# Optimization experiments

Measured on AMD Instinct MI355X. Metric: run time of the kernel, lower is better.

## Reference

```python
import math
import jax, jax.numpy as jnp
import numpy as np

EMB = 1024
HEADS = 16
HEAD_DIM = EMB // HEADS
FF = 4 * EMB
EPS = 1e-5


def gelu_tanh(x):
    c = math.sqrt(2.0 / math.pi)
    return 0.5 * x * (1.0 + jnp.tanh(c * (x + 0.044715 * x ** 3)))


def layernorm(x, scale, shift):
    mean = jnp.mean(x, axis=-1, keepdims=True)
    var = jnp.var(x, axis=-1, keepdims=True)
    return scale * (x - mean) / jnp.sqrt(var + EPS) + shift


def setup_inputs() -> dict:
    key = jax.random.key(0)
    ks = jax.random.split(key, 10)
    s = 0.02
    return {
        "x": jax.random.normal(ks[0], (2, 2048, EMB), dtype=jnp.float32),
        "Wq": jax.random.normal(ks[1], (EMB, EMB), dtype=jnp.float32) * s,
        "Wk": jax.random.normal(ks[2], (EMB, EMB), dtype=jnp.float32) * s,
        "Wv": jax.random.normal(ks[3], (EMB, EMB), dtype=jnp.float32) * s,
        "Wo": jax.random.normal(ks[4], (EMB, EMB), dtype=jnp.float32) * s,
        "bo": jnp.zeros((EMB,), dtype=jnp.float32),
        "W1": jax.random.normal(ks[5], (EMB, FF), dtype=jnp.float32) * s,
        "b1": jnp.zeros((FF,), dtype=jnp.float32),
        "W2": jax.random.normal(ks[6], (FF, EMB), dtype=jnp.float32) * s,
        "b2": jnp.zeros((EMB,), dtype=jnp.float32),
        "ln1_scale": jnp.ones((EMB,), dtype=jnp.float32),
        "ln1_shift": jnp.zeros((EMB,), dtype=jnp.float32),
        "ln2_scale": jnp.ones((EMB,), dtype=jnp.float32),
        "ln2_shift": jnp.zeros((EMB,), dtype=jnp.float32),
    }


def reference(x, Wq, Wk, Wv, Wo, bo, W1, b1, W2, b2,
              ln1_scale, ln1_shift, ln2_scale, ln2_shift):
    B, S, D = x.shape
    # --- pre-LN causal MHA ---
    h = layernorm(x, ln1_scale, ln1_shift)
    q = (h @ Wq).reshape(B, S, HEADS, HEAD_DIM).transpose(0, 2, 1, 3)  # [B,H,S,d]
    k = (h @ Wk).reshape(B, S, HEADS, HEAD_DIM).transpose(0, 2, 1, 3)
    v = (h @ Wv).reshape(B, S, HEADS, HEAD_DIM).transpose(0, 2, 1, 3)
    scores = jnp.einsum("bhqd,bhkd->bhqk", q, k)  # [B,H,S,S]
    causal = jnp.triu(jnp.ones((S, S), dtype=bool), k=1)
    scores = jnp.where(causal, -jnp.inf, scores)
    attn = jax.nn.softmax(scores / math.sqrt(HEAD_DIM), axis=-1)
    ctx = jnp.einsum("bhqk,bhkd->bhqd", attn, v)  # [B,H,S,d]
    ctx = ctx.transpose(0, 2, 1, 3).reshape(B, S, D)
    x = x + (ctx @ Wo + bo)
    # --- FFN ---
    h = layernorm(x, ln2_scale, ln2_shift)
    h = gelu_tanh(h @ W1 + b1) @ W2 + b2
    return x + h
```

## Files before the change

### kernel.cpp

```cpp
#include <hip/hip_runtime.h>
#include <hip/hip_bf16.h>
#include <math.h>

#define EMB 1024
#define HEADS 16
#define HEAD_DIM 64
#define FF_DIM 4096
#define SEQ 2048
#define BATCH 2
#define NTOK (BATCH * SEQ)
#define LN_EPS 1e-5f
#define QKV_N 3072
#define Q_PRESCALE 0.18033688011112042f

typedef __attribute__((ext_vector_type(8))) short s8v;
typedef __attribute__((ext_vector_type(4))) float f4v;

__device__ __forceinline__ unsigned short f2bf(float f) {
    union { __hip_bfloat16 h; unsigned short u; } cv;
    cv.h = __float2bfloat16(f);
    return cv.u;
}

__device__ __forceinline__ float fast_exp2(float x) {
#if __has_builtin(__builtin_amdgcn_exp2f)
    return __builtin_amdgcn_exp2f(x);
#else
    return exp2f(x);
#endif
}

__device__ __forceinline__ float gelu_f(float x) {
    const float c = 0.7978845608028654f;
    float x3 = x * x * x;
    return 0.5f * x * (1.0f + tanhf(c * (x + 0.044715f * x3)));
}

#define GLDS(gp, lp)                                                        \
    __builtin_amdgcn_global_load_lds(                                       \
        (const __attribute__((address_space(1))) void*)(gp),                \
        (__attribute__((address_space(3))) void*)(lp), 16, 0, 0)

__global__ __launch_bounds__(256) void ln_bf16_kernel(const float* __restrict__ x,
                                                      const float* __restrict__ scale,
                                                      const float* __restrict__ shift,
                                                      unsigned short* __restrict__ out) {
    int row = blockIdx.x;
    int tid = threadIdx.x;
    const float4 xv = ((const float4*)(x + (size_t)row * EMB))[tid];
    float s  = xv.x + xv.y + xv.z + xv.w;
    float ss = xv.x * xv.x + xv.y * xv.y + xv.z * xv.z + xv.w * xv.w;
    __shared__ float2 red[256];
    red[tid] = make_float2(s, ss);
    __syncthreads();
    for (int off = 128; off > 0; off >>= 1) {
        if (tid < off) {
            red[tid].x += red[tid + off].x;
            red[tid].y += red[tid + off].y;
        }
        __syncthreads();
    }
    float mean = red[0].x * (1.0f / EMB);
    float var  = red[0].y * (1.0f / EMB) - mean * mean;
    float rstd = rsqrtf(var + LN_EPS);
    float4 sc4 = ((const float4*)scale)[tid];
    float4 sh4 = ((const float4*)shift)[tid];
    ushort4 o;
    o.x = f2bf(sc4.x * (xv.x - mean) * rstd + sh4.x);
    o.y = f2bf(sc4.y * (xv.y - mean) * rstd + sh4.y);
    o.z = f2bf(sc4.z * (xv.z - mean) * rstd + sh4.z);
    o.w = f2bf(sc4.w * (xv.w - mean) * rstd + sh4.w);
    *(ushort4*)(out + (size_t)row * EMB + tid * 4) = o;
}

__global__ __launch_bounds__(256) void tconv_kernel(const float* __restrict__ W,
                                                    unsigned short* __restrict__ Wt,
                                                    int K, int N) {
    __shared__ float t[64][65];
    int n0 = blockIdx.x * 64, k0 = blockIdx.y * 64;
    int tid = threadIdx.x;
#pragma unroll
    for (int it = 0; it < 4; ++it) {
        int f = tid + it * 256;
        int r = f >> 4, c = (f & 15) * 4;
        float4 w = *(const float4*)(W + (size_t)(k0 + r) * N + n0 + c);
        t[r][c] = w.x; t[r][c + 1] = w.y; t[r][c + 2] = w.z; t[r][c + 3] = w.w;
    }
    __syncthreads();
#pragma unroll
    for (int it = 0; it < 4; ++it) {
        int f = tid + it * 256;
        int rn = f >> 4, ck = (f & 15) * 4;
        ushort4 o;
        o.x = f2bf(t[ck + 0][rn]);
        o.y = f2bf(t[ck + 1][rn]);
        o.z = f2bf(t[ck + 2][rn]);
        o.w = f2bf(t[ck + 3][rn]);
        *(ushort4*)(Wt + (size_t)(n0 + rn) * K + k0 + ck) = o;
    }
}

__global__ __launch_bounds__(256) void reduce_kernel(const float* __restrict__ p0,
                                                     const float* __restrict__ p1,
                                                     const float* __restrict__ bias,
                                                     const float* __restrict__ residual,
                                                     float* __restrict__ out) {
    size_t i4 = ((size_t)blockIdx.x * 256 + threadIdx.x) * 4;
    float4 a = *(const float4*)(p0 + i4);
    float4 b = *(const float4*)(p1 + i4);
    float4 r = *(const float4*)(residual + i4);
    int col = (int)(i4 & (EMB - 1));
    float4 bs = *(const float4*)(bias + col);
    float4 o;
    o.x = a.x + b.x + r.x + bs.x;
    o.y = a.y + b.y + r.y + bs.y;
    o.z = a.z + b.z + r.z + bs.z;
    o.w = a.w + b.w + r.w + bs.w;
    *(float4*)(out + i4) = o;
}

__global__ __launch_bounds__(256) void reduce_ln_kernel(const float* __restrict__ p0,
                                                        const float* __restrict__ p1,
                                                        const float* __restrict__ bias,
                                                        const float* __restrict__ residual,
                                                        float* __restrict__ x1,
                                                        const float* __restrict__ scale,
                                                        const float* __restrict__ shift,
                                                        unsigned short* __restrict__ out) {
    int row = blockIdx.x;
    int tid = threadIdx.x;
    size_t i4 = (size_t)row * EMB + tid * 4;
    float4 a = *(const float4*)(p0 + i4);
    float4 b = *(const float4*)(p1 + i4);
    float4 r = *(const float4*)(residual + i4);
    float4 bs = *(const float4*)(bias + tid * 4);
    float4 xv;
    xv.x = a.x + b.x + r.x + bs.x;
    xv.y = a.y + b.y + r.y + bs.y;
    xv.z = a.z + b.z + r.z + bs.z;
    xv.w = a.w + b.w + r.w + bs.w;
    *(float4*)(x1 + i4) = xv;

    float s  = xv.x + xv.y + xv.z + xv.w;
    float ss = xv.x * xv.x + xv.y * xv.y + xv.z * xv.z + xv.w * xv.w;
    __shared__ float2 red[256];
    red[tid] = make_float2(s, ss);
    __syncthreads();
    for (int off = 128; off > 0; off >>= 1) {
        if (tid < off) {
            red[tid].x += red[tid + off].x;
            red[tid].y += red[tid + off].y;
        }
        __syncthreads();
    }
    float mean = red[0].x * (1.0f / EMB);
    float var  = red[0].y * (1.0f / EMB) - mean * mean;
    float rstd = rsqrtf(var + LN_EPS);
    float4 sc4 = ((const float4*)scale)[tid];
    float4 sh4 = ((const float4*)shift)[tid];
    ushort4 o;
    o.x = f2bf(sc4.x * (xv.x - mean) * rstd + sh4.x);
    o.y = f2bf(sc4.y * (xv.y - mean) * rstd + sh4.y);
    o.z = f2bf(sc4.z * (xv.z - mean) * rstd + sh4.z);
    o.w = f2bf(sc4.w * (xv.w - mean) * rstd + sh4.w);
    *(ushort4*)(out + i4) = o;
}

__global__ __launch_bounds__(256) void gemm_bf16_kernel(
    const unsigned short* __restrict__ A,
    const unsigned short* __restrict__ Bt,
    float* __restrict__ Cf0,
    float* __restrict__ Cf1,
    unsigned short* __restrict__ Cb,
    int M, int N, int K, int Klen,
    const float* __restrict__ bias,
    const float* __restrict__ residual,
    int do_gelu, int qkv_mode,
    unsigned short* __restrict__ vt)
{
    __shared__ short As[2][4096];
    __shared__ short Bs[2][4096];

    int tid = threadIdx.x;
    int m0 = blockIdx.y * 128;
    int n0 = blockIdx.x * 128;
    int k0 = blockIdx.z * Klen;
    float* Cf = blockIdx.z ? Cf1 : Cf0;
    int wv = tid >> 6, lane = tid & 63;
    int wr = wv >> 1, wc = wv & 1;
    int quad = lane >> 4, ln = lane & 15;

    f4v acc[4][4];
#pragma unroll
    for (int i = 0; i < 4; ++i)
#pragma unroll
        for (int j = 0; j < 4; ++j) {
            f4v z = {0.f, 0.f, 0.f, 0.f};
            acc[i][j] = z;
        }

    int r0 = tid & 127;
    size_t Kby = (size_t)K << 1;
    const char* Ag0 = (const char*)A + (size_t)(m0 + r0) * Kby + (size_t)k0 * 2 + (tid >> 7) * 16;
    const char* Bg0 = (const char*)Bt + (size_t)(n0 + r0) * Kby + (size_t)k0 * 2 + (tid >> 7) * 16;

    int nIter = Klen >> 5;
    GLDS(Ag0, (char*)As[0] + tid * 16);
    GLDS(Ag0 + 32, (char*)As[0] + tid * 16 + 4096);
    GLDS(Bg0, (char*)Bs[0] + tid * 16);
    GLDS(Bg0 + 32, (char*)Bs[0] + tid * 16 + 4096);

    for (int it = 0; it < nIter; ++it) {
        __syncthreads();
        if (it + 1 < nIter) {
            int kb = (it + 1) << 6;
            char* Ad = (char*)As[(it + 1) & 1] + tid * 16;
            char* Bd = (char*)Bs[(it + 1) & 1] + tid * 16;
            GLDS(Ag0 + kb, Ad);
            GLDS(Ag0 + kb + 32, Ad + 4096);
            GLDS(Bg0 + kb, Bd);
            GLDS(Bg0 + kb + 32, Bd + 4096);
        }
        const short* Ab = As[it & 1];
        const short* Bb = Bs[it & 1];
        s8v af[4], bfr[4];
#pragma unroll
        for (int i = 0; i < 4; ++i)
            af[i] = *(const s8v*)(Ab + ((size_t)quad * 128 + wr * 64 + i * 16 + ln) * 8);
#pragma unroll
        for (int j = 0; j < 4; ++j)
            bfr[j] = *(const s8v*)(Bb + ((size_t)quad * 128 + wc * 64 + j * 16 + ln) * 8);
#pragma unroll
        for (int i = 0; i < 4; ++i)
#pragma unroll
            for (int j = 0; j < 4; ++j)
                acc[i][j] = __builtin_amdgcn_mfma_f32_16x16x32_bf16(af[i], bfr[j], acc[i][j], 0, 0, 0);
    }

    int cn  = n0 + wc * 64 + ln;
    int cm0 = m0 + wr * 64 + quad * 4;

    if (qkv_mode) {
        if (n0 < 2048) {
            float sc = (n0 < 1024) ? Q_PRESCALE : 1.0f;
#pragma unroll
            for (int j = 0; j < 4; ++j) {
                int gn = cn + j * 16;
#pragma unroll
                for (int i = 0; i < 4; ++i)
#pragma unroll
                    for (int r = 0; r < 4; ++r)
                        Cb[(size_t)(cm0 + i * 16 + r) * 2048 + gn] = f2bf(acc[i][j][r] * sc);
            }
        } else {
#pragma unroll
            for (int j = 0; j < 4; ++j) {
                int gn = cn + j * 16 - 2048;
#pragma unroll
                for (int i = 0; i < 4; ++i) {
                    int gm0 = cm0 + i * 16;
                    int bb = gm0 >> 11, s0 = gm0 & 2047;
                    ushort4 pk;
                    pk.x = f2bf(acc[i][j][0]);
                    pk.y = f2bf(acc[i][j][1]);
                    pk.z = f2bf(acc[i][j][2]);
                    pk.w = f2bf(acc[i][j][3]);
                    *(ushort4*)(vt + ((size_t)bb * 1024 + gn) * SEQ + s0) = pk;
                }
            }
        }
        return;
    }

#pragma unroll
    for (int j = 0; j < 4; ++j) {
        int gn = cn + j * 16;
        float bj = bias ? bias[gn] : 0.f;
#pragma unroll
        for (int i = 0; i < 4; ++i) {
#pragma unroll
            for (int r = 0; r < 4; ++r) {
                int gm = cm0 + i * 16 + r;
                float vv = acc[i][j][r] + bj;
                if (do_gelu) vv = gelu_f(vv);
                if (residual) vv += residual[(size_t)gm * N + gn];
                if (Cf) Cf[(size_t)gm * N + gn] = vv;
                else    Cb[(size_t)gm * N + gn] = f2bf(vv);
            }
        }
    }
}

__global__ __launch_bounds__(256) void flash_attn_mfma_kernel(
    const unsigned short* __restrict__ qk,
    const unsigned short* __restrict__ vt,
    unsigned short* __restrict__ ctx)
{
    int h  = blockIdx.x;
    int qt = (int)gridDim.y - 1 - (int)blockIdx.y;
    int b  = blockIdx.z;
    int tid = threadIdx.x;
    int w = tid >> 6, lane = tid & 63;
    int quad = lane >> 4, ln = lane & 15;

    __shared__ short Kb2[2][4096];
    __shared__ short Vb2[2][4096];
    __shared__ short Ps[4][32 * 72];

    size_t qrow0 = (size_t)b * SEQ + (size_t)qt * 128;
    int wrow0 = w * 32;

    s8v qf[2][2];
#pragma unroll
    for (int mb = 0; mb < 2; ++mb)
#pragma unroll
        for (int ks = 0; ks < 2; ++ks)
            qf[mb][ks] = *(const s8v*)(qk + (qrow0 + wrow0 + mb * 16 + ln) * 2048
                                          + h * 64 + ks * 32 + quad * 8);

    float l_part[2][4];
    f4v o[2][4];
#pragma unroll
    for (int mb = 0; mb < 2; ++mb) {
#pragma unroll
        for (int r = 0; r < 4; ++r) l_part[mb][r] = 0.f;
#pragma unroll
        for (int db = 0; db < 4; ++db) {
            f4v z = {0.f, 0.f, 0.f, 0.f};
            o[mb][db] = z;
        }
    }

    const unsigned short* kb_p = qk + (size_t)b * SEQ * 2048 + 1024 + h * 64;
    const unsigned short* vb_p = vt + ((size_t)b * 1024 + h * 64) * SEQ;
    short* Pw = Ps[w];

    int rr = tid & 63;
    const unsigned short* Kg0 = kb_p + (size_t)rr * 2048 + (tid >> 6) * 8;
    const unsigned short* Vg0 = vb_p + (size_t)rr * 2048 + (tid >> 6) * 8;

    int ktn = 2 * qt + 2;
    int ktmax_w = (qt * 128 + wrow0 + 31) >> 6;

    GLDS(Kg0, (char*)Kb2[0] + tid * 16);
    GLDS(Kg0 + 32, (char*)Kb2[0] + tid * 16 + 4096);
    GLDS(Vg0, (char*)Vb2[0] + tid * 16);
    GLDS(Vg0 + 32, (char*)Vb2[0] + tid * 16 + 4096);

    for (int kt = 0; kt < ktn; ++kt) {
        __syncthreads();
        if (kt + 1 < ktn) {
            int nb_ = (kt + 1) & 1;
            const unsigned short* ks_ = Kg0 + (size_t)(kt + 1) * 64 * 2048;
            const unsigned short* vs_ = Vg0 + (kt + 1) * 64;
            GLDS(ks_, (char*)Kb2[nb_] + tid * 16);
            GLDS(ks_ + 32, (char*)Kb2[nb_] + tid * 16 + 4096);
            GLDS(vs_, (char*)Vb2[nb_] + tid * 16);
            GLDS(vs_ + 32, (char*)Vb2[nb_] + tid * 16 + 4096);
        }
        if (kt > ktmax_w) continue;

        const short* Kl = Kb2[kt & 1];
        const short* Vl = Vb2[kt & 1];

        f4v s[2][4];
#pragma unroll
        for (int mb = 0; mb < 2; ++mb)
#pragma unroll
            for (int nb = 0; nb < 4; ++nb) {
                f4v z = {0.f, 0.f, 0.f, 0.f};
                s[mb][nb] = z;
            }
#pragma unroll
        for (int ks = 0; ks < 2; ++ks)
#pragma unroll
            for (int nb = 0; nb < 4; ++nb) {
                s8v kfr = *(const s8v*)(Kl + ((size_t)(ks * 4 + quad) * 64 + nb * 16 + ln) * 8);
#pragma unroll
                for (int mb = 0; mb < 2; ++mb)
                    s[mb][nb] = __builtin_amdgcn_mfma_f32_16x16x32_bf16(qf[mb][ks], kfr, s[mb][nb], 0, 0, 0);
            }

#pragma unroll
        for (int mb = 0; mb < 2; ++mb) {
#pragma unroll
            for (int r = 0; r < 4; ++r) {
                int rloc = mb * 16 + quad * 4 + r;
                int grow = qt * 128 + wrow0 + rloc;
                float p[4];
#pragma unroll
                for (int nb = 0; nb < 4; ++nb) {
                    int key = kt * 64 + nb * 16 + ln;
                    float e = fast_exp2(s[mb][nb][r]);
                    p[nb] = (key > grow) ? 0.f : e;
                }
                l_part[mb][r] += (p[0] + p[1]) + (p[2] + p[3]);
#pragma unroll
                for (int nb = 0; nb < 4; ++nb)
                    Pw[rloc * 72 + nb * 16 + ln] = f2bf(p[nb]);
            }
        }

#pragma unroll
        for (int ks = 0; ks < 2; ++ks) {
            s8v pf[2];
#pragma unroll
            for (int mb = 0; mb < 2; ++mb)
                pf[mb] = *(const s8v*)(Pw + (mb * 16 + ln) * 72 + ks * 32 + quad * 8);
#pragma unroll
            for (int db = 0; db < 4; ++db) {
                s8v vfr = *(const s8v*)(Vl + ((size_t)(ks * 4 + quad) * 64 + db * 16 + ln) * 8);
#pragma unroll
                for (int mb = 0; mb < 2; ++mb)
                    o[mb][db] = __builtin_amdgcn_mfma_f32_16x16x32_bf16(pf[mb], vfr, o[mb][db], 0, 0, 0);
            }
        }
    }

#pragma unroll
    for (int mb = 0; mb < 2; ++mb)
#pragma unroll
        for (int r = 0; r < 4; ++r) {
            float l = l_part[mb][r];
#pragma unroll
            for (int msk = 1; msk < 16; msk <<= 1)
                l += __shfl_xor(l, msk);
            float inv = 1.0f / l;
            size_t row = qrow0 + wrow0 + mb * 16 + quad * 4 + r;
#pragma unroll
            for (int db = 0; db < 4; ++db)
                ctx[row * EMB + h * 64 + db * 16 + ln] = f2bf(o[mb][db][r] * inv);
        }
}

extern "C" void kernel_launch(void* const* d_in, const int* in_sizes, int n_in,
                              void* d_out, int out_size, void* d_ws, size_t ws_size,
                              hipStream_t stream) {
    const float* x    = (const float*)d_in[0];
    const float* Wq   = (const float*)d_in[1];
    const float* Wk   = (const float*)d_in[2];
    const float* Wv   = (const float*)d_in[3];
    const float* Wo   = (const float*)d_in[4];
    const float* bo   = (const float*)d_in[5];
    const float* W1   = (const float*)d_in[6];
    const float* b1   = (const float*)d_in[7];
    const float* W2   = (const float*)d_in[8];
    const float* b2   = (const float*)d_in[9];
    const float* ln1s = (const float*)d_in[10];
    const float* ln1b = (const float*)d_in[11];
    const float* ln2s = (const float*)d_in[12];
    const float* ln2b = (const float*)d_in[13];
    float* out = (float*)d_out;

    const size_t MiB = 1024 * 1024;
    uint8_t* w8 = (uint8_t*)d_ws;
    unsigned short* Wqkv_t = (unsigned short*)(w8);
    unsigned short* Wo_t   = (unsigned short*)(w8 +  6 * MiB);
    unsigned short* W1_t   = (unsigned short*)(w8 +  8 * MiB);
    unsigned short* W2_t   = (unsigned short*)(w8 + 16 * MiB);
    unsigned short* act_bf = (unsigned short*)(w8 + 24 * MiB);
    unsigned short* qk_bf  = (unsigned short*)(w8 + 32 * MiB);
    unsigned short* vt     = (unsigned short*)(w8 + 48 * MiB);
    float*          p0a    = (float*)(w8 + 32 * MiB);
    float*          p1a    = (float*)(w8 + 48 * MiB);
    unsigned short* u_bf   = (unsigned short*)(w8 + 32 * MiB);
    float*          x1     = (float*)(w8 + 64 * MiB);
    float*          p0b    = (float*)(w8);
    float*          p1b    = (float*)(w8 + 80 * MiB);

    tconv_kernel<<<dim3(16, 16), 256, 0, stream>>>(Wq, Wqkv_t, EMB, EMB);
    tconv_kernel<<<dim3(16, 16), 256, 0, stream>>>(Wk, Wqkv_t + (size_t)1024 * EMB, EMB, EMB);
    tconv_kernel<<<dim3(16, 16), 256, 0, stream>>>(Wv, Wqkv_t + (size_t)2048 * EMB, EMB, EMB);
    tconv_kernel<<<dim3(16, 16), 256, 0, stream>>>(Wo, Wo_t, EMB, EMB);
    tconv_kernel<<<dim3(64, 16), 256, 0, stream>>>(W1, W1_t, EMB, FF_DIM);
    tconv_kernel<<<dim3(16, 64), 256, 0, stream>>>(W2, W2_t, FF_DIM, EMB);

    ln_bf16_kernel<<<NTOK, 256, 0, stream>>>(x, ln1s, ln1b, act_bf);

    gemm_bf16_kernel<<<dim3(QKV_N / 128, NTOK / 128, 1), 256, 0, stream>>>(
        act_bf, Wqkv_t, nullptr, nullptr, qk_bf, NTOK, QKV_N, EMB, EMB,
        nullptr, nullptr, 0, 1, vt);

    flash_attn_mfma_kernel<<<dim3(HEADS, SEQ / 128, BATCH), 256, 0, stream>>>(qk_bf, vt, act_bf);

    gemm_bf16_kernel<<<dim3(EMB / 128, NTOK / 128, 2), 256, 0, stream>>>(
        act_bf, Wo_t, p0a, p1a, nullptr, NTOK, EMB, EMB, 512,
        nullptr, nullptr, 0, 0, nullptr);
    reduce_ln_kernel<<<NTOK, 256, 0, stream>>>(p0a, p1a, bo, x, x1, ln2s, ln2b, act_bf);

    gemm_bf16_kernel<<<dim3(FF_DIM / 128, NTOK / 128, 1), 256, 0, stream>>>(
        act_bf, W1_t, nullptr, nullptr, u_bf, NTOK, FF_DIM, EMB, EMB,
        b1, nullptr, 1, 0, nullptr);

    gemm_bf16_kernel<<<dim3(EMB / 128, NTOK / 128, 2), 256, 0, stream>>>(
        u_bf, W2_t, p0b, p1b, nullptr, NTOK, EMB, FF_DIM, 2048,
        nullptr, nullptr, 0, 0, nullptr);
    reduce_kernel<<<(NTOK * EMB) / 1024, 256, 0, stream>>>(p0b, p1b, b2, x1, out);
}
```

Measured before the change: 493.3 us.

## Add 128x256 wide GEMM for QKV/FFN1, merge weight transposes, specialize split-K GEMM

```diff
diff --git a/kernel.cpp b/kernel.cpp
--- a/kernel.cpp
+++ b/kernel.cpp
@@ -73,12 +73,11 @@
     *(ushort4*)(out + (size_t)row * EMB + tid * 4) = o;
 }
 
-__global__ __launch_bounds__(256) void tconv_kernel(const float* __restrict__ W,
-                                                    unsigned short* __restrict__ Wt,
-                                                    int K, int N) {
+__device__ __forceinline__ void tconv_tile(const float* __restrict__ W,
+                                           unsigned short* __restrict__ Wt,
+                                           int K, int N, int bx, int by, int tid) {
     __shared__ float t[64][65];
-    int n0 = blockIdx.x * 64, k0 = blockIdx.y * 64;
-    int tid = threadIdx.x;
+    int n0 = bx * 64, k0 = by * 64;
 #pragma unroll
     for (int it = 0; it < 4; ++it) {
         int f = tid + it * 256;
@@ -98,6 +97,22 @@
         o.w = f2bf(t[ck + 3][rn]);
         *(ushort4*)(Wt + (size_t)(n0 + rn) * K + k0 + ck) = o;
     }
+}
+
+__global__ __launch_bounds__(256) void tconv_all_kernel(
+    const float* __restrict__ Wq, const float* __restrict__ Wk,
+    const float* __restrict__ Wv, const float* __restrict__ Wo,
+    const float* __restrict__ W1, const float* __restrict__ W2,
+    unsigned short* __restrict__ Wqkv_t, unsigned short* __restrict__ Wo_t,
+    unsigned short* __restrict__ W1_t, unsigned short* __restrict__ W2_t) {
+    int b = blockIdx.x;
+    int tid = threadIdx.x;
+    if (b < 256)        tconv_tile(Wq, Wqkv_t,                      EMB, EMB,    b & 15, b >> 4, tid);
+    else if (b < 512)   tconv_tile(Wk, Wqkv_t + (size_t)1024 * EMB, EMB, EMB,    (b - 256) & 15, (b - 256) >> 4, tid);
+    else if (b < 768)   tconv_tile(Wv, Wqkv_t + (size_t)2048 * EMB, EMB, EMB,    (b - 512) & 15, (b - 512) >> 4, tid);
+    else if (b < 1024)  tconv_tile(Wo, Wo_t,                        EMB, EMB,    (b - 768) & 15, (b - 768) >> 4, tid);
+    else if (b < 2048)  tconv_tile(W1, W1_t,                        EMB, FF_DIM, (b - 1024) & 63, (b - 1024) >> 6, tid);
+    else                tconv_tile(W2, W2_t,                        FF_DIM, EMB, (b - 2048) & 15, (b - 2048) >> 4, tid);
 }
 
 __global__ __launch_bounds__(256) void reduce_kernel(const float* __restrict__ p0,
@@ -166,17 +181,130 @@
     *(ushort4*)(out + i4) = o;
 }
 
+__global__ __launch_bounds__(256, 2) void gemm_wide_kernel(
+    const unsigned short* __restrict__ A,
+    const unsigned short* __restrict__ Bt,
+    unsigned short* __restrict__ Cb,
+    int M, int N, int K,
+    const float* __restrict__ bias,
+    int do_gelu, int qkv_mode,
+    unsigned short* __restrict__ vt)
+{
+    __shared__ short As[2][4096];
+    __shared__ short Bs[2][8192];
+
+    int tid = threadIdx.x;
+    int m0 = blockIdx.y * 128;
+    int n0 = blockIdx.x * 256;
+    int wv = tid >> 6, lane = tid & 63;
+    int wr = wv >> 1, wc = wv & 1;
+    int quad = lane >> 4, ln = lane & 15;
+
+    f4v acc[4][8];
+#pragma unroll
+    for (int i = 0; i < 4; ++i)
+#pragma unroll
+        for (int j = 0; j < 8; ++j) {
+            f4v z = {0.f, 0.f, 0.f, 0.f};
+            acc[i][j] = z;
+        }
+
+    size_t Kby = (size_t)K << 1;
+    const char* Ag0 = (const char*)A + (size_t)(m0 + (tid & 127)) * Kby + (tid >> 7) * 16;
+    const char* Bg0 = (const char*)Bt + (size_t)(n0 + tid) * Kby;
+
+    int nIter = K >> 5;
+    GLDS(Ag0, (char*)As[0] + tid * 16);
+    GLDS(Ag0 + 32, (char*)As[0] + tid * 16 + 4096);
+#pragma unroll
+    for (int i = 0; i < 4; ++i)
+        GLDS(Bg0 + i * 16, (char*)Bs[0] + tid * 16 + i * 4096);
+
+    for (int it = 0; it < nIter; ++it) {
+        __syncthreads();
+        if (it + 1 < nIter) {
+            int kb = (it + 1) << 6;
+            char* Ad = (char*)As[(it + 1) & 1] + tid * 16;
+            char* Bd = (char*)Bs[(it + 1) & 1] + tid * 16;
+            GLDS(Ag0 + kb, Ad);
+            GLDS(Ag0 + kb + 32, Ad + 4096);
+#pragma unroll
+            for (int i = 0; i < 4; ++i)
+                GLDS(Bg0 + kb + i * 16, Bd + i * 4096);
+        }
+        const short* Ab = As[it & 1];
+        const short* Bb = Bs[it & 1];
+        s8v af[4], bfr[8];
+#pragma unroll
+        for (int i = 0; i < 4; ++i)
+            af[i] = *(const s8v*)(Ab + ((size_t)quad * 128 + wr * 64 + i * 16 + ln) * 8);
+#pragma unroll
+        for (int j = 0; j < 8; ++j)
+            bfr[j] = *(const s8v*)(Bb + ((size_t)quad * 256 + wc * 128 + j * 16 + ln) * 8);
+#pragma unroll
+        for (int i = 0; i < 4; ++i)
+#pragma unroll
+            for (int j = 0; j < 8; ++j)
+                acc[i][j] = __builtin_amdgcn_mfma_f32_16x16x32_bf16(af[i], bfr[j], acc[i][j], 0, 0, 0);
+    }
+
+    int cn  = n0 + wc * 128 + ln;
+    int cm0 = m0 + wr * 64 + quad * 4;
+
+    if (qkv_mode) {
+        if (n0 < 2048) {
+            float sc = (n0 < 1024) ? Q_PRESCALE : 1.0f;
+#pragma unroll
+            for (int j = 0; j < 8; ++j) {
+                int gn = cn + j * 16;
+#pragma unroll
+                for (int i = 0; i < 4; ++i)
+#pragma unroll
+                    for (int r = 0; r < 4; ++r)
+                        Cb[(size_t)(cm0 + i * 16 + r) * 2048 + gn] = f2bf(acc[i][j][r] * sc);
+            }
+        } else {
+#pragma unroll
+            for (int j = 0; j < 8; ++j) {
+                int gn = cn + j * 16 - 2048;
+#pragma unroll
+                for (int i = 0; i < 4; ++i) {
+                    int gm0 = cm0 + i * 16;
+                    int bb = gm0 >> 11, s0 = gm0 & 2047;
+                    ushort4 pk;
+                    pk.x = f2bf(acc[i][j][0]);
+                    pk.y = f2bf(acc[i][j][1]);
+                    pk.z = f2bf(acc[i][j][2]);
+                    pk.w = f2bf(acc[i][j][3]);
+                    *(ushort4*)(vt + ((size_t)bb * 1024 + gn) * SEQ + s0) = pk;
+                }
+            }
+        }
+        return;
+    }
+
+#pragma unroll
+    for (int j = 0; j < 8; ++j) {
+        int gn = cn + j * 16;
+        float bj = bias ? bias[gn] : 0.f;
+#pragma unroll
+        for (int i = 0; i < 4; ++i) {
+#pragma unroll
+            for (int r = 0; r < 4; ++r) {
+                float vv = acc[i][j][r] + bj;
+                if (do_gelu) vv = gelu_f(vv);
+                Cb[(size_t)(cm0 + i * 16 + r) * N + gn] = f2bf(vv);
+            }
+        }
+    }
+}
+
 __global__ __launch_bounds__(256) void gemm_bf16_kernel(
     const unsigned short* __restrict__ A,
     const unsigned short* __restrict__ Bt,
     float* __restrict__ Cf0,
     float* __restrict__ Cf1,
-    unsigned short* __restrict__ Cb,
-    int M, int N, int K, int Klen,
-    const float* __restrict__ bias,
-    const float* __restrict__ residual,
-    int do_gelu, int qkv_mode,
-    unsigned short* __restrict__ vt)
+    int M, int N, int K, int Klen)
 {
     __shared__ short As[2][4096];
     __shared__ short Bs[2][4096];
@@ -239,55 +367,14 @@
 
     int cn  = n0 + wc * 64 + ln;
     int cm0 = m0 + wr * 64 + quad * 4;
-
-    if (qkv_mode) {
-        if (n0 < 2048) {
-            float sc = (n0 < 1024) ? Q_PRESCALE : 1.0f;
-#pragma unroll
-            for (int j = 0; j < 4; ++j) {
-                int gn = cn + j * 16;
-#pragma unroll
-                for (int i = 0; i < 4; ++i)
-#pragma unroll
-                    for (int r = 0; r < 4; ++r)
-                        Cb[(size_t)(cm0 + i * 16 + r) * 2048 + gn] = f2bf(acc[i][j][r] * sc);
-            }
-        } else {
-#pragma unroll
-            for (int j = 0; j < 4; ++j) {
-                int gn = cn + j * 16 - 2048;
-#pragma unroll
-                for (int i = 0; i < 4; ++i) {
-                    int gm0 = cm0 + i * 16;
-                    int bb = gm0 >> 11, s0 = gm0 & 2047;
-                    ushort4 pk;
-                    pk.x = f2bf(acc[i][j][0]);
-                    pk.y = f2bf(acc[i][j][1]);
-                    pk.z = f2bf(acc[i][j][2]);
-                    pk.w = f2bf(acc[i][j][3]);
-                    *(ushort4*)(vt + ((size_t)bb * 1024 + gn) * SEQ + s0) = pk;
-                }
-            }
-        }
-        return;
-    }
-
 #pragma unroll
     for (int j = 0; j < 4; ++j) {
         int gn = cn + j * 16;
-        float bj = bias ? bias[gn] : 0.f;
-#pragma unroll
-        for (int i = 0; i < 4; ++i) {
-#pragma unroll
-            for (int r = 0; r < 4; ++r) {
-                int gm = cm0 + i * 16 + r;
-                float vv = acc[i][j][r] + bj;
-                if (do_gelu) vv = gelu_f(vv);
-                if (residual) vv += residual[(size_t)gm * N + gn];
-                if (Cf) Cf[(size_t)gm * N + gn] = vv;
-                else    Cb[(size_t)gm * N + gn] = f2bf(vv);
-            }
-        }
+#pragma unroll
+        for (int i = 0; i < 4; ++i)
+#pragma unroll
+            for (int r = 0; r < 4; ++r)
+                Cf[(size_t)(cm0 + i * 16 + r) * N + gn] = acc[i][j][r];
     }
 }
 
@@ -468,32 +555,24 @@
     float*          p0b    = (float*)(w8);
     float*          p1b    = (float*)(w8 + 80 * MiB);
 
-    tconv_kernel<<<dim3(16, 16), 256, 0, stream>>>(Wq, Wqkv_t, EMB, EMB);
-    tconv_kernel<<<dim3(16, 16), 256, 0, stream>>>(Wk, Wqkv_t + (size_t)1024 * EMB, EMB, EMB);
-    tconv_kernel<<<dim3(16, 16), 256, 0, stream>>>(Wv, Wqkv_t + (size_t)2048 * EMB, EMB, EMB);
-    tconv_kernel<<<dim3(16, 16), 256, 0, stream>>>(Wo, Wo_t, EMB, EMB);
-    tconv_kernel<<<dim3(64, 16), 256, 0, stream>>>(W1, W1_t, EMB, FF_DIM);
-    tconv_kernel<<<dim3(16, 64), 256, 0, stream>>>(W2, W2_t, FF_DIM, EMB);
+    tconv_all_kernel<<<3072, 256, 0, stream>>>(Wq, Wk, Wv, Wo, W1, W2,
+                                               Wqkv_t, Wo_t, W1_t, W2_t);
 
     ln_bf16_kernel<<<NTOK, 256, 0, stream>>>(x, ln1s, ln1b, act_bf);
 
-    gemm_bf16_kernel<<<dim3(QKV_N / 128, NTOK / 128, 1), 256, 0, stream>>>(
-        act_bf, Wqkv_t, nullptr, nullptr, qk_bf, NTOK, QKV_N, EMB, EMB,
-        nullptr, nullptr, 0, 1, vt);
+    gemm_wide_kernel<<<dim3(QKV_N / 256, NTOK / 128), 256, 0, stream>>>(
+        act_bf, Wqkv_t, qk_bf, NTOK, QKV_N, EMB, nullptr, 0, 1, vt);
 
     flash_attn_mfma_kernel<<<dim3(HEADS, SEQ / 128, BATCH), 256, 0, stream>>>(qk_bf, vt, act_bf);
 
     gemm_bf16_kernel<<<dim3(EMB / 128, NTOK / 128, 2), 256, 0, stream>>>(
-        act_bf, Wo_t, p0a, p1a, nullptr, NTOK, EMB, EMB, 512,
-        nullptr, nullptr, 0, 0, nullptr);
+        act_bf, Wo_t, p0a, p1a, NTOK, EMB, EMB, 512);
     reduce_ln_kernel<<<NTOK, 256, 0, stream>>>(p0a, p1a, bo, x, x1, ln2s, ln2b, act_bf);
 
-    gemm_bf16_kernel<<<dim3(FF_DIM / 128, NTOK / 128, 1), 256, 0, stream>>>(
-        act_bf, W1_t, nullptr, nullptr, u_bf, NTOK, FF_DIM, EMB, EMB,
-        b1, nullptr, 1, 0, nullptr);
+    gemm_wide_kernel<<<dim3(FF_DIM / 256, NTOK / 128), 256, 0, stream>>>(
+        act_bf, W1_t, u_bf, NTOK, FF_DIM, EMB, b1, 1, 0, nullptr);
 
     gemm_bf16_kernel<<<dim3(EMB / 128, NTOK / 128, 2), 256, 0, stream>>>(
-        u_bf, W2_t, p0b, p1b, nullptr, NTOK, EMB, FF_DIM, 2048,
-        nullptr, nullptr, 0, 0, nullptr);
+        u_bf, W2_t, p0b, p1b, NTOK, EMB, FF_DIM, 2048);
     reduce_kernel<<<(NTOK * EMB) / 1024, 256, 0, stream>>>(p0b, p1b, b2, x1, out);
 }
```

Result: faster. 469.6 us (-4.8%).
